# Kernel optimization log

Hardware: AMD Instinct MI355X
Metric: run time of the kernel (lower is better)

Reference implementation:

```python
import jax, jax.numpy as jnp
import numpy as np

N_SITES = 1024
HIDDEN = 64
BATCH = 16384  # num_samples


def setup_inputs() -> dict:
    key = jax.random.key(0)
    ks = jax.random.split(key, 7)
    H = HIDDEN
    s = 0.1  # weight init scale
    return {
        "u": jax.random.uniform(ks[0], (BATCH, N_SITES), jnp.float32),  # bernoulli noise
        "w_ih": jax.random.normal(ks[1], (3 * H, 1), jnp.float32) * s,   # gate order [r,z,n]
        "w_hh": jax.random.normal(ks[2], (3 * H, H), jnp.float32) * s,
        "b_ih": jax.random.normal(ks[3], (3 * H,), jnp.float32) * s,
        "b_hh": jax.random.normal(ks[4], (3 * H,), jnp.float32) * s,
        "head_w": jax.random.normal(ks[5], (1, H), jnp.float32) * s,
        "head_b": jax.random.normal(ks[6], (1,), jnp.float32) * s,
    }


def reference(u, w_ih, w_hh, b_ih, b_hh, head_w, head_b):
    # sequential over sites via lax.scan. PyTorch GRU cell math, gates [r,z,n].
    H = w_hh.shape[1]
    B = u.shape[0]
    w_ih_vec = w_ih[:, 0]  # input_size == 1 -> [3H]

    def step(carry, u_t):
        h, prev = carry  # h: [B,H], prev: [B] previous sampled bit
        gx = prev[:, None] * w_ih_vec[None, :] + b_ih  # [B,3H]
        gh = h @ w_hh.T + b_hh                          # [B,3H]
        r = jax.nn.sigmoid(gx[:, :H] + gh[:, :H])
        z = jax.nn.sigmoid(gx[:, H:2 * H] + gh[:, H:2 * H])
        n = jnp.tanh(gx[:, 2 * H:] + r * gh[:, 2 * H:])
        h_new = (1.0 - z) * n + z * h
        logit = h_new @ head_w[0] + head_b[0]  # [B]
        p = jax.nn.sigmoid(logit)
        bit = (u_t < p).astype(h.dtype)  # bernoulli(p) via pre-drawn uniform
        return (h_new, bit), bit

    h0 = jnp.zeros((B, H), u.dtype)
    prev0 = jnp.zeros((B,), u.dtype)  # torch starts with prev = 0
    _, bits = jax.lax.scan(step, (h0, prev0), u.T)  # bits: [n_sites, B]
    return bits.T.astype(jnp.int32)  # [B, n_sites], matches samples.long()
```

## Files before the change

### kernel.cpp

```cpp
#include <hip/hip_runtime.h>

#define NS 1024
#define NH 64
#define NB 16384


__device__ __forceinline__ float xexp(float x) {
  x = fminf(x, 88.3762626647950f);
  x = fmaxf(x, -88.3762626647949f);
  float fx = floorf(__fadd_rn(__fmul_rn(x, 1.44269504088896341f), 0.5f));
  x = __fsub_rn(x, __fmul_rn(fx, 0.693359375f));
  x = __fsub_rn(x, __fmul_rn(fx, -2.12194440e-4f));
  float z = __fmul_rn(x, x);
  float y = 1.9875691500e-4f;
  y = __fadd_rn(__fmul_rn(y, x), 1.3981999507e-3f);
  y = __fadd_rn(__fmul_rn(y, x), 8.3334519073e-3f);
  y = __fadd_rn(__fmul_rn(y, x), 4.1665795894e-2f);
  y = __fadd_rn(__fmul_rn(y, x), 1.6666665459e-1f);
  y = __fadd_rn(__fmul_rn(y, x), 5.0000001201e-1f);
  y = __fadd_rn(__fmul_rn(y, z), x);
  y = __fadd_rn(y, 1.0f);
  int n = (int)fx;
  float p2n = __int_as_float((n + 127) << 23);
  return __fmul_rn(y, p2n);
}

__device__ __forceinline__ float xsigmoid(float x) {
  float e = xexp(-x);
  return __fdiv_rn(1.0f, __fadd_rn(1.0f, e));
}

__device__ __forceinline__ float xtanh(float x) {
  float xc = fminf(fmaxf(x, -7.90531110763549805f), 7.90531110763549805f);
  float s = __fmul_rn(xc, xc);
  float p = -2.76076847742355e-16f;
  p = __fadd_rn(__fmul_rn(p, s), 2.00018790482477e-13f);
  p = __fadd_rn(__fmul_rn(p, s), -8.60467152213735e-11f);
  p = __fadd_rn(__fmul_rn(p, s), 5.12229709037114e-08f);
  p = __fadd_rn(__fmul_rn(p, s), 1.48572235717979e-05f);
  p = __fadd_rn(__fmul_rn(p, s), 6.37261928875436e-04f);
  p = __fadd_rn(__fmul_rn(p, s), 4.89352455891786e-03f);
  float num = __fmul_rn(xc, p);
  float q = 1.19825839466702e-06f;
  q = __fadd_rn(__fmul_rn(q, s), 1.18534705686654e-04f);
  q = __fadd_rn(__fmul_rn(q, s), 2.26843463243900e-03f);
  q = __fadd_rn(__fmul_rn(q, s), 4.89352518554385e-03f);
  float rat = __fdiv_rn(num, q);
  return (fabsf(x) < 0.0004f) ? x : rat;
}

__global__ __launch_bounds__(256, 2) void gru_sample_kernel(
    const float* __restrict__ u, const float* __restrict__ w_ih,
    const float* __restrict__ w_hh, const float* __restrict__ b_ih,
    const float* __restrict__ b_hh, const float* __restrict__ head_w,
    const float* __restrict__ head_b, int* __restrict__ out) {
  const int lane = threadIdx.x & 63;
  const int wv = threadIdx.x >> 6;
  const int row = blockIdx.x * 4 + wv;
  if (row >= NB) return;

  __shared__ float hbuf[4][NH];

  float w_r[NH], w_z[NH], w_n[NH];
#pragma unroll
  for (int kq = 0; kq < 16; ++kq) {
    float4 a = *(const float4*)&w_hh[(size_t)(lane)*NH + kq * 4];
    float4 b = *(const float4*)&w_hh[(size_t)(64 + lane) * NH + kq * 4];
    float4 c = *(const float4*)&w_hh[(size_t)(128 + lane) * NH + kq * 4];
    w_r[kq * 4 + 0] = a.x; w_r[kq * 4 + 1] = a.y; w_r[kq * 4 + 2] = a.z; w_r[kq * 4 + 3] = a.w;
    w_z[kq * 4 + 0] = b.x; w_z[kq * 4 + 1] = b.y; w_z[kq * 4 + 2] = b.z; w_z[kq * 4 + 3] = b.w;
    w_n[kq * 4 + 0] = c.x; w_n[kq * 4 + 1] = c.y; w_n[kq * 4 + 2] = c.z; w_n[kq * 4 + 3] = c.w;
  }
  const float bih_r = b_ih[lane], bih_z = b_ih[64 + lane], bih_n = b_ih[128 + lane];
  const float bhh_r = b_hh[lane], bhh_z = b_hh[64 + lane], bhh_n = b_hh[128 + lane];
  const float wih_r = w_ih[lane], wih_z = w_ih[64 + lane], wih_n = w_ih[128 + lane];
  const float hw = head_w[lane];
  const float hb = head_b[0];

  const float* urow = u + (size_t)row * NS;
  int* orow = out + (size_t)row * NS;

  float h = 0.0f, prev = 0.0f;
  hbuf[wv][lane] = 0.0f;

  float u_cur = urow[lane];
  for (int c = 0; c < 16; ++c) {
    float u_next = (c < 15) ? urow[(c + 1) * 64 + lane] : 0.0f;
    float mybit = 0.0f;
    for (int tt = 0; tt < 64; ++tt) {
      float acc_r = 0.0f, acc_z = 0.0f, acc_n = 0.0f;
#pragma unroll
      for (int kq = 0; kq < 16; ++kq) {
        float4 hv = *(const float4*)&hbuf[wv][kq * 4];
        acc_r = fmaf(hv.x, w_r[kq * 4 + 0], acc_r);
        acc_r = fmaf(hv.y, w_r[kq * 4 + 1], acc_r);
        acc_r = fmaf(hv.z, w_r[kq * 4 + 2], acc_r);
        acc_r = fmaf(hv.w, w_r[kq * 4 + 3], acc_r);
        acc_z = fmaf(hv.x, w_z[kq * 4 + 0], acc_z);
        acc_z = fmaf(hv.y, w_z[kq * 4 + 1], acc_z);
        acc_z = fmaf(hv.z, w_z[kq * 4 + 2], acc_z);
        acc_z = fmaf(hv.w, w_z[kq * 4 + 3], acc_z);
        acc_n = fmaf(hv.x, w_n[kq * 4 + 0], acc_n);
        acc_n = fmaf(hv.y, w_n[kq * 4 + 1], acc_n);
        acc_n = fmaf(hv.z, w_n[kq * 4 + 2], acc_n);
        acc_n = fmaf(hv.w, w_n[kq * 4 + 3], acc_n);
      }
      float gh_r = __fadd_rn(acc_r, bhh_r);
      float gh_z = __fadd_rn(acc_z, bhh_z);
      float gh_n = __fadd_rn(acc_n, bhh_n);
      float gx_r = __fadd_rn(__fmul_rn(prev, wih_r), bih_r);
      float gx_z = __fadd_rn(__fmul_rn(prev, wih_z), bih_z);
      float gx_n = __fadd_rn(__fmul_rn(prev, wih_n), bih_n);
      float r = xsigmoid(__fadd_rn(gx_r, gh_r));
      float z = xsigmoid(__fadd_rn(gx_z, gh_z));
      float n = xtanh(__fadd_rn(gx_n, __fmul_rn(r, gh_n)));
      float hn = __fadd_rn(__fmul_rn(__fsub_rn(1.0f, z), n), __fmul_rn(z, h));
      h = hn;
      hbuf[wv][lane] = h;

      float P = __fmul_rn(h, hw);
      float s = __fadd_rn(P, __shfl(P, lane + 16));
      s = __fadd_rn(s, __shfl(P, lane + 32));
      s = __fadd_rn(s, __shfl(P, lane + 48));
      s = __fadd_rn(s, __shfl(s, lane + 8));
      s = __fadd_rn(s, __shfl(s, lane + 4));
      s = __fadd_rn(s, __shfl(s, lane + 2));
      s = __fadd_rn(s, __shfl(s, lane + 1));
      float logit = __fadd_rn(__shfl(s, 0), hb);
      float p = xsigmoid(logit);

      float u_t = __shfl(u_cur, tt);
      float bit = (u_t < p) ? 1.0f : 0.0f;
      prev = bit;
      mybit = (lane == tt) ? bit : mybit;
    }
    orow[c * 64 + lane] = (int)mybit;
    u_cur = u_next;
  }
}

extern "C" void kernel_launch(void* const* d_in, const int* in_sizes, int n_in,
                              void* d_out, int out_size, void* d_ws, size_t ws_size,
                              hipStream_t stream) {
  const float* u = (const float*)d_in[0];
  const float* w_ih = (const float*)d_in[1];
  const float* w_hh = (const float*)d_in[2];
  const float* b_ih = (const float*)d_in[3];
  const float* b_hh = (const float*)d_in[4];
  const float* head_w = (const float*)d_in[5];
  const float* head_b = (const float*)d_in[6];
  int* out = (int*)d_out;
  dim3 grid(NB / 4), block(256);
  gru_sample_kernel<<<grid, block, 0, stream>>>(u, w_ih, w_hh, b_ih, b_hh,
                                                head_w, head_b, out);
}
```

Measured before the change: 8.697 ms.

## Move n-gate weights to LDS and launch one wavefront per block

The n-gate recurrent weights move from registers into shared memory as float4 per lane, which cuts per-thread register use from about 192 weight floats to 128. Each block now holds a single 64-thread wavefront handling one batch row. The input-gate term is precomputed as w_ih+b_ih and picked by the integer previous bit instead of a multiply-add. The aim is more resident waves per SIMD to hide the serial latency of each step, at the cost of extra LDS reads in the inner dot-product loop.

```diff
diff --git a/kernel.cpp b/kernel.cpp
--- a/kernel.cpp
+++ b/kernel.cpp
@@ -49,74 +49,75 @@
   return (fabsf(x) < 0.0004f) ? x : rat;
 }
 
-__global__ __launch_bounds__(256, 2) void gru_sample_kernel(
+__global__ __launch_bounds__(64, 2) void gru_sample_kernel(
     const float* __restrict__ u, const float* __restrict__ w_ih,
     const float* __restrict__ w_hh, const float* __restrict__ b_ih,
     const float* __restrict__ b_hh, const float* __restrict__ head_w,
     const float* __restrict__ head_b, int* __restrict__ out) {
-  const int lane = threadIdx.x & 63;
-  const int wv = threadIdx.x >> 6;
-  const int row = blockIdx.x * 4 + wv;
-  if (row >= NB) return;
+  const int lane = threadIdx.x;
+  const int row = blockIdx.x;
 
-  __shared__ float hbuf[4][NH];
+  __shared__ float4 wnq[16][NH];
+  __shared__ float hb_[NH];
 
-  float w_r[NH], w_z[NH], w_n[NH];
+  float w_r[NH], w_z[NH];
 #pragma unroll
   for (int kq = 0; kq < 16; ++kq) {
     float4 a = *(const float4*)&w_hh[(size_t)(lane)*NH + kq * 4];
     float4 b = *(const float4*)&w_hh[(size_t)(64 + lane) * NH + kq * 4];
-    float4 c = *(const float4*)&w_hh[(size_t)(128 + lane) * NH + kq * 4];
     w_r[kq * 4 + 0] = a.x; w_r[kq * 4 + 1] = a.y; w_r[kq * 4 + 2] = a.z; w_r[kq * 4 + 3] = a.w;
     w_z[kq * 4 + 0] = b.x; w_z[kq * 4 + 1] = b.y; w_z[kq * 4 + 2] = b.z; w_z[kq * 4 + 3] = b.w;
-    w_n[kq * 4 + 0] = c.x; w_n[kq * 4 + 1] = c.y; w_n[kq * 4 + 2] = c.z; w_n[kq * 4 + 3] = c.w;
+  }
+#pragma unroll
+  for (int k4 = 0; k4 < 16; ++k4) {
+    wnq[k4][lane] = *(const float4*)&w_hh[(size_t)(128 + lane) * NH + 4 * k4];
   }
   const float bih_r = b_ih[lane], bih_z = b_ih[64 + lane], bih_n = b_ih[128 + lane];
   const float bhh_r = b_hh[lane], bhh_z = b_hh[64 + lane], bhh_n = b_hh[128 + lane];
-  const float wih_r = w_ih[lane], wih_z = w_ih[64 + lane], wih_n = w_ih[128 + lane];
+  const float sum_r = __fadd_rn(w_ih[lane], bih_r);
+  const float sum_z = __fadd_rn(w_ih[64 + lane], bih_z);
+  const float sum_n = __fadd_rn(w_ih[128 + lane], bih_n);
   const float hw = head_w[lane];
   const float hb = head_b[0];
 
   const float* urow = u + (size_t)row * NS;
   int* orow = out + (size_t)row * NS;
 
-  float h = 0.0f, prev = 0.0f;
-  hbuf[wv][lane] = 0.0f;
+  float h = 0.0f;
+  int prev = 0;
+  hb_[lane] = 0.0f;
 
   float u_cur = urow[lane];
   for (int c = 0; c < 16; ++c) {
     float u_next = (c < 15) ? urow[(c + 1) * 64 + lane] : 0.0f;
-    float mybit = 0.0f;
+    int mybit = 0;
     for (int tt = 0; tt < 64; ++tt) {
-      float acc_r = 0.0f, acc_z = 0.0f, acc_n = 0.0f;
+      float ar = 0.0f, az = 0.0f, an = 0.0f;
 #pragma unroll
       for (int kq = 0; kq < 16; ++kq) {
-        float4 hv = *(const float4*)&hbuf[wv][kq * 4];
-        acc_r = fmaf(hv.x, w_r[kq * 4 + 0], acc_r);
-        acc_r = fmaf(hv.y, w_r[kq * 4 + 1], acc_r);
-        acc_r = fmaf(hv.z, w_r[kq * 4 + 2], acc_r);
-        acc_r = fmaf(hv.w, w_r[kq * 4 + 3], acc_r);
-        acc_z = fmaf(hv.x, w_z[kq * 4 + 0], acc_z);
-        acc_z = fmaf(hv.y, w_z[kq * 4 + 1], acc_z);
-        acc_z = fmaf(hv.z, w_z[kq * 4 + 2], acc_z);
-        acc_z = fmaf(hv.w, w_z[kq * 4 + 3], acc_z);
-        acc_n = fmaf(hv.x, w_n[kq * 4 + 0], acc_n);
-        acc_n = fmaf(hv.y, w_n[kq * 4 + 1], acc_n);
-        acc_n = fmaf(hv.z, w_n[kq * 4 + 2], acc_n);
-        acc_n = fmaf(hv.w, w_n[kq * 4 + 3], acc_n);
+        float4 hv = *(const float4*)&hb_[kq * 4];
+        float4 wn = wnq[kq][lane];
+        ar = fmaf(hv.x, w_r[kq * 4 + 0], ar);
+        ar = fmaf(hv.y, w_r[kq * 4 + 1], ar);
+        ar = fmaf(hv.z, w_r[kq * 4 + 2], ar);
+        ar = fmaf(hv.w, w_r[kq * 4 + 3], ar);
+        az = fmaf(hv.x, w_z[kq * 4 + 0], az);
+        az = fmaf(hv.y, w_z[kq * 4 + 1], az);
+        az = fmaf(hv.z, w_z[kq * 4 + 2], az);
+        az = fmaf(hv.w, w_z[kq * 4 + 3], az);
+        an = fmaf(hv.x, wn.x, an);
+        an = fmaf(hv.y, wn.y, an);
+        an = fmaf(hv.z, wn.z, an);
+        an = fmaf(hv.w, wn.w, an);
       }
-      float gh_r = __fadd_rn(acc_r, bhh_r);
-      float gh_z = __fadd_rn(acc_z, bhh_z);
-      float gh_n = __fadd_rn(acc_n, bhh_n);
-      float gx_r = __fadd_rn(__fmul_rn(prev, wih_r), bih_r);
-      float gx_z = __fadd_rn(__fmul_rn(prev, wih_z), bih_z);
-      float gx_n = __fadd_rn(__fmul_rn(prev, wih_n), bih_n);
-      float r = xsigmoid(__fadd_rn(gx_r, gh_r));
-      float z = xsigmoid(__fadd_rn(gx_z, gh_z));
-      float n = xtanh(__fadd_rn(gx_n, __fmul_rn(r, gh_n)));
-      float hn = __fadd_rn(__fmul_rn(__fsub_rn(1.0f, z), n), __fmul_rn(z, h));
-      h = hn;
-      hbuf[wv][lane] = h;
+      float gh_r = __fadd_rn(ar, bhh_r);
+      float gh_z = __fadd_rn(az, bhh_z);
+      float gh_n = __fadd_rn(an, bhh_n);
+      float r = xsigmoid(__fadd_rn(prev ? sum_r : bih_r, gh_r));
+      float z = xsigmoid(__fadd_rn(prev ? sum_z : bih_z, gh_z));
+      float n = xtanh(__fadd_rn(prev ? sum_n : bih_n, __fmul_rn(r, gh_n)));
+      h = __fadd_rn(__fmul_rn(__fsub_rn(1.0f, z), n), __fmul_rn(z, h));
+      hb_[lane] = h;
 
       float P = __fmul_rn(h, hw);
       float s = __fadd_rn(P, __shfl(P, lane + 16));
@@ -130,11 +131,11 @@
       float p = xsigmoid(logit);
 
       float u_t = __shfl(u_cur, tt);
-      float bit = (u_t < p) ? 1.0f : 0.0f;
-      prev = bit;
-      mybit = (lane == tt) ? bit : mybit;
+      int b = (u_t < p) ? 1 : 0;
+      prev = b;
+      mybit = (lane == tt) ? b : mybit;
     }
-    orow[c * 64 + lane] = (int)mybit;
+    orow[c * 64 + lane] = mybit;
     u_cur = u_next;
   }
 }
@@ -150,7 +151,7 @@
   const float* head_w = (const float*)d_in[5];
   const float* head_b = (const float*)d_in[6];
   int* out = (int*)d_out;
-  dim3 grid(NB / 4), block(256);
+  dim3 grid(NB), block(64);
   gru_sample_kernel<<<grid, block, 0, stream>>>(u, w_ih, w_hh, b_ih, b_hh,
                                                 head_w, head_b, out);
 }
```

Result: faster. 8.401 ms (-3.4%).
